# Kernel tuning notes

Hardware: AMD Instinct MI355X
Metric: run time of the kernel (lower is better)

## Reference

```python
import jax, jax.numpy as jnp
import numpy as np

P = 8          # patch_num_in == patch_num_out
R = 16         # patch_resolution (pixels per patch side)
C = 2          # dim_channel
D = 512        # dim_token
NH = 8         # nhead
DFF = 2048     # dim_feedforward
L = 6          # num_layers
PAIRS = 5      # demo_num
BS = 8
HW = P * R     # 128
S = PAIRS * 2 * P * P  # 640 tokens
EPS = 1e-5


def _patchify(x):
    # x: (N, c, H, W) -> (N, P*P, c*R*R)
    N, c, H, W = x.shape
    x = x.reshape(N, c, P, R, P, R).transpose(0, 2, 4, 1, 3, 5)
    return x.reshape(N, P * P, c * R * R)


def _depatchify(x, c):
    # x: (N, P*P, c*R*R) -> (N, c, P*R, P*R)
    N = x.shape[0]
    x = x.reshape(N, P, P, c, R, R).transpose(0, 3, 1, 4, 2, 5)
    return x.reshape(N, c, P * R, P * R)


def _ln(x, s, b):
    mu = jnp.mean(x, axis=-1, keepdims=True)
    var = jnp.mean(jnp.square(x - mu), axis=-1, keepdims=True)
    return (x - mu) * jax.lax.rsqrt(var + EPS) * s + b


def _block_lowtri_additive_mask(seq_len):
    blk = jnp.arange(seq_len) // (P * P)  # alternating init/end blocks of size P*P
    allowed = blk[:, None] >= blk[None, :]
    return jnp.where(allowed, 0.0, -jnp.inf).astype(jnp.float32)


def setup_inputs() -> dict:
    key = jax.random.key(0)
    ks = jax.random.split(key, 20)
    s = 0.02
    f32 = jnp.float32
    inp = {
        "init": jax.random.normal(ks[0], (BS, PAIRS, C, HW, HW), f32),
        "end": jax.random.normal(ks[1], (BS, PAIRS, C, HW, HW), f32),
        "c_mask": jnp.ones((BS, C), dtype=bool),
        "pre_W": (jax.random.normal(ks[2], (D, C * R * R), f32) * s),
        "pre_b": jnp.zeros((D,), f32),
        "post_W": (jax.random.normal(ks[3], (C * R * R, D), f32) * s),
        "post_b": jnp.zeros((C * R * R,), f32),
        "patch_pos": jax.random.normal(ks[4], (P * P, D), f32),
        "func_pos": jax.random.normal(ks[5], (PAIRS * 2, D), f32),
        "Wqkv": (jax.random.normal(ks[6], (L, 3 * D, D), f32) * s),
        "bqkv": jnp.zeros((L, 3 * D), f32),
        "Wo": (jax.random.normal(ks[7], (L, D, D), f32) * s),
        "bo": jnp.zeros((L, D), f32),
        "ln1_s": jnp.ones((L, D), f32),
        "ln1_b": jnp.zeros((L, D), f32),
        "ln2_s": jnp.ones((L, D), f32),
        "ln2_b": jnp.zeros((L, D), f32),
        "W1": (jax.random.normal(ks[8], (L, DFF, D), f32) * s),
        "b1": jnp.zeros((L, DFF), f32),
        "W2": (jax.random.normal(ks[9], (L, D, DFF), f32) * s),
        "b2": jnp.zeros((L, D), f32),
    }
    return inp


def _forward(init, end, pre_W, pre_b, post_W, post_b, patch_pos, func_pos,
             Wqkv, bqkv, Wo, bo, ln1_s, ln1_b, ln2_s, ln2_b, W1, b1, W2, b2):
    bs, pairs = init.shape[0], init.shape[1]
    # interleave (init, end) per pair: (bs, pairs, 2, c, h, w)
    x = jnp.concatenate([init[:, :, None], end[:, :, None]], axis=2)
    f = x.reshape(-1, C, HW, HW)
    f = _patchify(f)                                    # (N, P*P, C*R*R)
    f = f @ pre_W.T + pre_b                             # (N, P*P, D)
    f = f + patch_pos                                   # patch pos encoding
    f = f.reshape(bs, pairs * 2, P * P, D)
    f = f + func_pos[: pairs * 2][None, :, None, :]     # func pos encoding
    seq = pairs * 2 * P * P
    f = f.reshape(bs, seq, D)

    amask = _block_lowtri_additive_mask(seq)            # (S, S) additive
    dh = D // NH
    scale = 1.0 / np.sqrt(dh).astype(np.float32)

    for l in range(L):
        qkv = f @ Wqkv[l].T + bqkv[l]                   # (bs, S, 3D)
        q, k, v = jnp.split(qkv, 3, axis=-1)
        q = q.reshape(bs, seq, NH, dh).transpose(0, 2, 1, 3)
        k = k.reshape(bs, seq, NH, dh).transpose(0, 2, 1, 3)
        v = v.reshape(bs, seq, NH, dh).transpose(0, 2, 1, 3)
        scores = jnp.einsum('bhqd,bhkd->bhqk', q, k) * scale + amask
        attn = jax.nn.softmax(scores, axis=-1)
        o = jnp.einsum('bhqk,bhkd->bhqd', attn, v)
        o = o.transpose(0, 2, 1, 3).reshape(bs, seq, D)
        o = o @ Wo[l].T + bo[l]
        f = _ln(f + o, ln1_s[l], ln1_b[l])              # post-norm (PyTorch default)
        ff = jax.nn.gelu(f @ W1[l].T + b1[l], approximate=False) @ W2[l].T + b2[l]
        f = _ln(f + ff, ln2_s[l], ln2_b[l])

    f = f.reshape(bs, pairs, 2, P * P, D)[:, :, 0]      # read prediction off init slots
    f = f @ post_W.T + post_b                           # (bs, pairs, P*P, C*R*R)
    f = f.reshape(bs * pairs, P * P, C * R * R)
    f = _depatchify(f, C)
    return f.reshape(bs, pairs, C, HW, HW)


def reference(init, end, c_mask, pre_W, pre_b, post_W, post_b, patch_pos, func_pos,
              Wqkv, bqkv, Wo, bo, ln1_s, ln1_b, ln2_s, ln2_b, W1, b1, W2, b2):
    # c_mask is unpacked but unused by the original forward
    return _forward(init, end, pre_W, pre_b, post_W, post_b, patch_pos, func_pos,
                    Wqkv, bqkv, Wo, bo, ln1_s, ln1_b, ln2_s, ln2_b, W1, b1, W2, b2)
```

## Files before the change

kernel.cpp:

```cpp
#include <hip/hip_runtime.h>
#include <hip/hip_bf16.h>

#define BSZ 8
#define PAIRS 5
#define NCH 2
#define HWP 128
#define PP 64
#define DIM 512
#define NHEAD 8
#define DHEAD 64
#define DFF 2048
#define NLAYER 6
#define SEQ 640
#define NTOK (BSZ * SEQ)
#define FIN 10
#define MPOST (BSZ * PAIRS * PP)

typedef unsigned short u16;
typedef __bf16 bf16_t;
typedef __attribute__((ext_vector_type(8))) __bf16 bf16x8;
typedef __attribute__((ext_vector_type(4))) float f32x4;
#define MFMA16(a, b, c) __builtin_amdgcn_mfma_f32_16x16x32_bf16(a, b, c, 0, 0, 0)

__device__ __forceinline__ u16 f2b(float x) {
  unsigned u = __float_as_uint(x);
  return (u16)((u + 0x7fffu + ((u >> 16) & 1u)) >> 16);
}

__device__ __forceinline__ float gelu_t(float x) {
  float y = 0.7978845608f * (x + 0.044715f * x * x * x);
  y = fminf(fmaxf(y, -10.f), 10.f);
  float e = __expf(2.f * y);
  return 0.5f * x * (1.f + (e - 1.f) / (e + 1.f));
}

__device__ __forceinline__ void dma16(const u16* g, void* l) {
  __builtin_amdgcn_global_load_lds(
      (const __attribute__((address_space(1))) void*)g,
      (__attribute__((address_space(3))) void*)l, 16, 0, 0);
}

#define W_QKV (3 * DIM * DIM)
#define W_O (DIM * DIM)
#define W_1 (DFF * DIM)
#define OFF_O W_QKV
#define OFF_1 (W_QKV + W_O)
#define OFF_2 (W_QKV + W_O + W_1)
#define W_ALL (W_QKV + W_O + 2 * W_1)
#define PREPOST (2 * DIM * DIM)
#define N_CVT (PREPOST + NLAYER * W_ALL)

__global__ __launch_bounds__(256) void k_cvt_all(const float* __restrict__ preW,
                                                 const float* __restrict__ postW,
                                                 const float* __restrict__ wq,
                                                 const float* __restrict__ wo,
                                                 const float* __restrict__ w1,
                                                 const float* __restrict__ w2,
                                                 u16* __restrict__ dst) {
  int i = blockIdx.x * 256 + threadIdx.x;
  float v;
  if (i < DIM * DIM) v = preW[i];
  else if (i < PREPOST) v = postW[i - DIM * DIM];
  else {
    int j = i - PREPOST;
    int l = j / W_ALL;
    int r = j - l * W_ALL;
    if (r < OFF_O) v = wq[(size_t)l * W_QKV + r];
    else if (r < OFF_1) v = wo[(size_t)l * W_O + r - OFF_O];
    else if (r < OFF_2) v = w1[(size_t)l * W_1 + r - OFF_1];
    else v = w2[(size_t)l * W_1 + r - OFF_2];
  }
  dst[i] = f2b(v);
}

__global__ __launch_bounds__(256) void k_patchify(const float* __restrict__ init,
                                                  const float* __restrict__ endp,
                                                  u16* __restrict__ A) {
  int i = blockIdx.x * 256 + threadIdx.x;
  int d = i & 511;
  int g = i >> 9;
  int p = g & 63;
  int fi = (g >> 6) % FIN;
  int b = g / SEQ;
  int e = fi & 1;
  int pr = fi >> 1;
  int c = d >> 8;
  int r1 = (d >> 4) & 15;
  int r2 = d & 15;
  int row = ((p >> 3) << 4) + r1;
  int col = ((p & 7) << 4) + r2;
  const float* src = e ? endp : init;
  size_t off = ((size_t)((b * PAIRS + pr) * NCH + c) << 14) + (size_t)row * HWP + col;
  A[i] = f2b(src[off]);
}

template <int NT, int MODE>
__global__ __launch_bounds__(256) void k_mma(const u16* __restrict__ A,
                                             const u16* __restrict__ B,
                                             const float* __restrict__ bias,
                                             u16* __restrict__ outB,
                                             float* __restrict__ outP,
                                             float* __restrict__ outF,
                                             const float* __restrict__ pp,
                                             const float* __restrict__ fp,
                                             int M, int N, int K, int Kblk, int act) {
  constexpr int FJ = NT / 32;
  constexpr int NC = (4 + NT / 16) / 4;
  __shared__ __align__(16) bf16_t As[2][64][32];
  __shared__ __align__(16) bf16_t Bs[2][NT][32];
  const int t = threadIdx.x;
  const int w = t >> 6, lane = t & 63, quad = lane >> 4, l16 = lane & 15;
  int bx = blockIdx.x, by = blockIdx.y;
  if ((gridDim.y & 7) == 0) {
    int lin = bx + gridDim.x * by;
    int YT = gridDim.y >> 3;
    int xcd = lin & 7, slot = lin >> 3;
    by = xcd * YT + slot % YT;
    bx = slot / YT;
  }
  const int row0 = by << 6, col0 = bx * NT;
  const size_t kOff = (size_t)blockIdx.z * Kblk;
  const int mB = (w & 1) << 5;
  const int nB = (w >> 1) * (NT / 2);

  const u16* aP[4];
#pragma unroll
  for (int c = 0; c < 4; ++c) {
    int r = row0 + c * 16 + (lane >> 2);
    int g = r;
    if (MODE == 3) {
      int p = r & 63, pr = (r >> 6) % PAIRS, b = r / (PAIRS * PP);
      g = b * SEQ + pr * 128 + p;
    }
    aP[c] = A + (size_t)g * K + kOff + ((lane & 3) << 3);
  }
  const u16* bP = B + (size_t)(col0 + (lane >> 2)) * K + kOff + ((lane & 3) << 3);

  f32x4 acc[2][FJ];
#pragma unroll
  for (int i = 0; i < 2; ++i)
#pragma unroll
    for (int j = 0; j < FJ; ++j) acc[i][j] = (f32x4){0.f, 0.f, 0.f, 0.f};

  auto stage = [&](int bu, int kk) {
#pragma unroll
    for (int s = 0; s < NC; ++s) {
      int c = NC * w + s;
      if (c < 4) dma16(aP[c] + kk, &As[bu][c * 16][0]);
      else dma16(bP + (size_t)((c - 4) * 16) * K + kk, &Bs[bu][(c - 4) * 16][0]);
    }
  };

  const int iters = Kblk >> 5;
  stage(0, 0);
  for (int it = 0; it < iters; ++it) {
    const int cur = it & 1;
    if (it > 0) asm volatile("s_barrier" ::: "memory");
    const bool more = (it + 1 < iters);
    if (more) stage(cur ^ 1, (it + 1) << 5);
    if (more) {
      if (NC == 3) asm volatile("s_waitcnt vmcnt(3)" ::: "memory");
      else asm volatile("s_waitcnt vmcnt(2)" ::: "memory");
    } else {
      asm volatile("s_waitcnt vmcnt(0)" ::: "memory");
    }
    asm volatile("s_barrier" ::: "memory");
    bf16x8 af[2], bfr[FJ];
#pragma unroll
    for (int i = 0; i < 2; ++i)
      af[i] = *(const bf16x8*)&As[cur][mB + i * 16 + l16][quad * 8];
#pragma unroll
    for (int j = 0; j < FJ; ++j)
      bfr[j] = *(const bf16x8*)&Bs[cur][nB + j * 16 + l16][quad * 8];
#pragma unroll
    for (int i = 0; i < 2; ++i)
#pragma unroll
      for (int j = 0; j < FJ; ++j) acc[i][j] = MFMA16(af[i], bfr[j], acc[i][j]);
  }

#pragma unroll
  for (int i = 0; i < 2; ++i)
#pragma unroll
    for (int reg = 0; reg < 4; ++reg) {
      int m = row0 + mB + i * 16 + quad * 4 + reg;
#pragma unroll
      for (int j = 0; j < FJ; ++j) {
        int n = col0 + nB + j * 16 + l16;
        float v = acc[i][j][reg];
        if (MODE == 0) {
          v += bias[n];
          if (act) v = gelu_t(v);
          outB[(size_t)m * N + n] = f2b(v);
        } else if (MODE == 1) {
          outP[(size_t)blockIdx.z * M * N + (size_t)m * N + n] = v;
        } else if (MODE == 2) {
          int p = m & 63, fi = (m >> 6) % FIN;
          v += bias[n] + pp[p * DIM + n] + fp[fi * DIM + n];
          outF[(size_t)m * N + n] = v;
          outB[(size_t)m * N + n] = f2b(v);
        } else {
          v += bias[n];
          int p = m & 63, pr = (m >> 6) % PAIRS, b = m / (PAIRS * PP);
          int c = n >> 8, r1 = (n >> 4) & 15, r2 = n & 15;
          int row = ((p >> 3) << 4) + r1, col = ((p & 7) << 4) + r2;
          size_t off = ((size_t)((b * PAIRS + pr) * NCH + c) << 14) +
                       (size_t)row * HWP + col;
          outF[off] = v;
        }
      }
    }
}

__global__ __launch_bounds__(256) void k_attn(const u16* __restrict__ qkv,
                                              u16* __restrict__ o) {
  __shared__ bf16_t Qs[64][72];
  __shared__ bf16_t Ks[64][72];
  __shared__ bf16_t Vs[64][72];
  __shared__ bf16_t Ps[64][72];
  const int t = threadIdx.x;
  const int w = t >> 6, lane = t & 63, quad = lane >> 4, l16 = lane & 15;
  const int qblk = blockIdx.x, h = blockIdx.y, b = blockIdx.z;
  const int q0 = qblk << 6;
  const u16* base = qkv + (size_t)b * SEQ * (3 * DIM);
  const int sr = t >> 2;
  const int sd = (t & 3) << 4;
  {
    const u16* qp = base + (size_t)(q0 + sr) * (3 * DIM) + h * DHEAD + sd;
    *(bf16x8*)&Qs[sr][sd] = *(const bf16x8*)(const void*)qp;
    *(bf16x8*)&Qs[sr][sd + 8] = *(const bf16x8*)(const void*)(qp + 8);
  }
  __syncthreads();
  bf16x8 aQ0 = *(const bf16x8*)&Qs[w * 16 + l16][quad * 8];
  bf16x8 aQ1 = *(const bf16x8*)&Qs[w * 16 + l16][32 + quad * 8];
  f32x4 accO[4];
#pragma unroll
  for (int j = 0; j < 4; ++j) accO[j] = (f32x4){0.f, 0.f, 0.f, 0.f};
  float mSt[4] = {-1e30f, -1e30f, -1e30f, -1e30f};
  float lSt[4] = {0.f, 0.f, 0.f, 0.f};
  const int ntile = qblk + 1;
  for (int kt = 0; kt < ntile; ++kt) {
    {
      const u16* kp = base + (size_t)(kt * 64 + sr) * (3 * DIM) + DIM + h * DHEAD + sd;
      *(bf16x8*)&Ks[sr][sd] = *(const bf16x8*)(const void*)kp;
      *(bf16x8*)&Ks[sr][sd + 8] = *(const bf16x8*)(const void*)(kp + 8);
      const u16* vp = base + (size_t)(kt * 64 + sr) * (3 * DIM) + 2 * DIM + h * DHEAD + sd;
      bf16x8 v0 = *(const bf16x8*)(const void*)vp;
      bf16x8 v1 = *(const bf16x8*)(const void*)(vp + 8);
#pragma unroll
      for (int e = 0; e < 8; ++e) Vs[sd + e][sr] = v0[e];
#pragma unroll
      for (int e = 0; e < 8; ++e) Vs[sd + 8 + e][sr] = v1[e];
    }
    __syncthreads();
    f32x4 s[4];
#pragma unroll
    for (int j = 0; j < 4; ++j) {
      bf16x8 b0 = *(const bf16x8*)&Ks[j * 16 + l16][quad * 8];
      bf16x8 b1 = *(const bf16x8*)&Ks[j * 16 + l16][32 + quad * 8];
      s[j] = (f32x4){0.f, 0.f, 0.f, 0.f};
      s[j] = MFMA16(aQ0, b0, s[j]);
      s[j] = MFMA16(aQ1, b1, s[j]);
      s[j] *= 0.125f;
    }
#pragma unroll
    for (int reg = 0; reg < 4; ++reg) {
      float mx = fmaxf(fmaxf(s[0][reg], s[1][reg]), fmaxf(s[2][reg], s[3][reg]));
      mx = fmaxf(mx, __shfl_xor(mx, 1));
      mx = fmaxf(mx, __shfl_xor(mx, 2));
      mx = fmaxf(mx, __shfl_xor(mx, 4));
      mx = fmaxf(mx, __shfl_xor(mx, 8));
      float mNew = fmaxf(mSt[reg], mx);
      float alpha = __expf(mSt[reg] - mNew);
      mSt[reg] = mNew;
      float rs = 0.f;
#pragma unroll
      for (int j = 0; j < 4; ++j) {
        float p = __expf(s[j][reg] - mNew);
        s[j][reg] = p;
        rs += p;
      }
      rs += __shfl_xor(rs, 1);
      rs += __shfl_xor(rs, 2);
      rs += __shfl_xor(rs, 4);
      rs += __shfl_xor(rs, 8);
      lSt[reg] = lSt[reg] * alpha + rs;
#pragma unroll
      for (int j = 0; j < 4; ++j) accO[j][reg] *= alpha;
    }
#pragma unroll
    for (int j = 0; j < 4; ++j)
#pragma unroll
      for (int reg = 0; reg < 4; ++reg)
        *(u16*)&Ps[w * 16 + quad * 4 + reg][j * 16 + l16] = f2b(s[j][reg]);
    __syncthreads();
    bf16x8 aP0 = *(const bf16x8*)&Ps[w * 16 + l16][quad * 8];
    bf16x8 aP1 = *(const bf16x8*)&Ps[w * 16 + l16][32 + quad * 8];
#pragma unroll
    for (int jd = 0; jd < 4; ++jd) {
      bf16x8 b0 = *(const bf16x8*)&Vs[jd * 16 + l16][quad * 8];
      bf16x8 b1 = *(const bf16x8*)&Vs[jd * 16 + l16][32 + quad * 8];
      accO[jd] = MFMA16(aP0, b0, accO[jd]);
      accO[jd] = MFMA16(aP1, b1, accO[jd]);
    }
    __syncthreads();
  }
#pragma unroll
  for (int reg = 0; reg < 4; ++reg) {
    float inv = 1.0f / lSt[reg];
    int row = q0 + w * 16 + quad * 4 + reg;
#pragma unroll
    for (int jd = 0; jd < 4; ++jd)
      o[((size_t)(b * SEQ + row)) * DIM + h * DHEAD + jd * 16 + l16] =
          f2b(accO[jd][reg] * inv);
  }
}

__global__ __launch_bounds__(256) void k_red_ln(const float* __restrict__ part, int KS,
                                                const float* __restrict__ bias,
                                                float* __restrict__ f,
                                                u16* __restrict__ fb,
                                                const float* __restrict__ s,
                                                const float* __restrict__ bvec) {
  const int row = blockIdx.x;
  const int t = threadIdx.x;
  const size_t base = (size_t)row * DIM;
  float x0 = f[base + t] + bias[t];
  float x1 = f[base + t + 256] + bias[t + 256];
  for (int z = 0; z < KS; ++z) {
    x0 += part[(size_t)z * NTOK * DIM + base + t];
    x1 += part[(size_t)z * NTOK * DIM + base + t + 256];
  }
  float sum = x0 + x1;
  float sq = x0 * x0 + x1 * x1;
#pragma unroll
  for (int off = 32; off; off >>= 1) {
    sum += __shfl_xor(sum, off);
    sq += __shfl_xor(sq, off);
  }
  __shared__ float rs[4], rq[4];
  const int w = t >> 6, lane = t & 63;
  if (lane == 0) { rs[w] = sum; rq[w] = sq; }
  __syncthreads();
  float tot = rs[0] + rs[1] + rs[2] + rs[3];
  float tq2 = rq[0] + rq[1] + rq[2] + rq[3];
  float mu = tot * (1.0f / 512.0f);
  float var = tq2 * (1.0f / 512.0f) - mu * mu;
  float rstd = rsqrtf(var + 1e-5f);
  float v0 = (x0 - mu) * rstd * s[t] + bvec[t];
  float v1 = (x1 - mu) * rstd * s[t + 256] + bvec[t + 256];
  f[base + t] = v0;
  f[base + t + 256] = v1;
  fb[base + t] = f2b(v0);
  fb[base + t + 256] = f2b(v1);
}

extern "C" void kernel_launch(void* const* d_in, const int* in_sizes, int n_in,
                              void* d_out, int out_size, void* d_ws, size_t ws_size,
                              hipStream_t stream) {
  const float* init = (const float*)d_in[0];
  const float* endp = (const float*)d_in[1];
  const float* pre_W = (const float*)d_in[3];
  const float* pre_b = (const float*)d_in[4];
  const float* post_W = (const float*)d_in[5];
  const float* post_b = (const float*)d_in[6];
  const float* patch_pos = (const float*)d_in[7];
  const float* func_pos = (const float*)d_in[8];
  const float* Wqkv = (const float*)d_in[9];
  const float* bqkv = (const float*)d_in[10];
  const float* Wo = (const float*)d_in[11];
  const float* bo = (const float*)d_in[12];
  const float* ln1_s = (const float*)d_in[13];
  const float* ln1_b = (const float*)d_in[14];
  const float* ln2_s = (const float*)d_in[15];
  const float* ln2_b = (const float*)d_in[16];
  const float* W1 = (const float*)d_in[17];
  const float* b1 = (const float*)d_in[18];
  const float* W2 = (const float*)d_in[19];
  const float* b2 = (const float*)d_in[20];
  float* out = (float*)d_out;

  char* p = (char*)d_ws;
  float* buf_f = (float*)p;    p += (size_t)NTOK * DIM * 4;
  u16* buf_fb = (u16*)p;       p += (size_t)NTOK * DIM * 2;
  u16* buf_attn = (u16*)p;     p += (size_t)NTOK * DIM * 2;
  u16* shared_b = (u16*)p;     p += (size_t)NTOK * DFF * 2;
  u16* wAll = (u16*)p;         p += (size_t)N_CVT * 2;
  float* partial = (float*)p;
  u16* buf_patch = shared_b;
  u16* buf_qkv = shared_b;
  u16* buf_hid = shared_b;
  u16* wPre = wAll;
  u16* wPost = wAll + DIM * DIM;
  u16* wL = wAll + PREPOST;

  dim3 blk(256);
  const int elems = NTOK * DIM;

  k_cvt_all<<<N_CVT / 256, blk, 0, stream>>>(pre_W, post_W, Wqkv, Wo, W1, W2, wAll);
  k_patchify<<<elems / 256, blk, 0, stream>>>(init, endp, buf_patch);
  k_mma<64, 2><<<dim3(8, 80, 1), blk, 0, stream>>>(
      buf_patch, wPre, pre_b, buf_fb, nullptr, buf_f, patch_pos, func_pos,
      NTOK, DIM, DIM, DIM, 0);

  for (int l = 0; l < NLAYER; ++l) {
    u16* wB = wL + (size_t)l * W_ALL;
    k_mma<128, 0><<<dim3(12, 80, 1), blk, 0, stream>>>(
        buf_fb, wB, bqkv + (size_t)l * 3 * DIM, buf_qkv, nullptr, nullptr, nullptr,
        nullptr, NTOK, 3 * DIM, DIM, DIM, 0);
    k_attn<<<dim3(SEQ / 64, NHEAD, BSZ), blk, 0, stream>>>(buf_qkv, buf_attn);
    k_mma<64, 1><<<dim3(8, 80, 1), blk, 0, stream>>>(
        buf_attn, wB + OFF_O, nullptr, nullptr, partial, nullptr, nullptr, nullptr,
        NTOK, DIM, DIM, DIM, 0);
    k_red_ln<<<NTOK, blk, 0, stream>>>(partial, 1, bo + (size_t)l * DIM, buf_f,
                                       buf_fb, ln1_s + (size_t)l * DIM,
                                       ln1_b + (size_t)l * DIM);
    k_mma<128, 0><<<dim3(16, 80, 1), blk, 0, stream>>>(
        buf_fb, wB + OFF_1, b1 + (size_t)l * DFF, buf_hid, nullptr, nullptr, nullptr,
        nullptr, NTOK, DFF, DIM, DIM, 1);
    k_mma<64, 1><<<dim3(8, 80, 2), blk, 0, stream>>>(
        buf_hid, wB + OFF_2, nullptr, nullptr, partial, nullptr, nullptr, nullptr,
        NTOK, DIM, DFF, DFF / 2, 0);
    k_red_ln<<<NTOK, blk, 0, stream>>>(partial, 2, b2 + (size_t)l * DIM, buf_f,
                                       buf_fb, ln2_s + (size_t)l * DIM,
                                       ln2_b + (size_t)l * DIM);
  }

  k_mma<64, 3><<<dim3(8, 40, 1), blk, 0, stream>>>(
      buf_fb, wPost, post_b, nullptr, nullptr, out, nullptr, nullptr,
      MPOST, DIM, DIM, DIM, 0);
}
```

Measured before the change: 972.6 us.

## Triple-buffer GEMM loads, prefetch attention K/V, vectorize weight cast, drop FFN2 split-K

The GEMM mainloop goes from double to triple buffering in LDS, issuing async loads two K-steps ahead with adjusted vmcnt waits, to hide more global latency. The attention kernel now prefetches the next K/V tile into registers while the current tile is processed. The weight conversion kernel handles 8 elements per thread with vector loads and stores. The FFN down-projection drops its 2-way split-K, so there are fewer partials to reduce but only half as many blocks for that GEMM.

```diff
diff --git a/kernel.cpp b/kernel.cpp
--- a/kernel.cpp
+++ b/kernel.cpp
@@ -19,6 +19,7 @@
 typedef unsigned short u16;
 typedef __bf16 bf16_t;
 typedef __attribute__((ext_vector_type(8))) __bf16 bf16x8;
+typedef __attribute__((ext_vector_type(8))) unsigned short u16x8;
 typedef __attribute__((ext_vector_type(4))) float f32x4;
 #define MFMA16(a, b, c) __builtin_amdgcn_mfma_f32_16x16x32_bf16(a, b, c, 0, 0, 0)
 
@@ -57,20 +58,26 @@
                                                  const float* __restrict__ w1,
                                                  const float* __restrict__ w2,
                                                  u16* __restrict__ dst) {
-  int i = blockIdx.x * 256 + threadIdx.x;
-  float v;
-  if (i < DIM * DIM) v = preW[i];
-  else if (i < PREPOST) v = postW[i - DIM * DIM];
+  size_t i = ((size_t)blockIdx.x * 256 + threadIdx.x) * 8;
+  const float* src;
+  size_t off;
+  if (i < DIM * DIM) { src = preW; off = i; }
+  else if (i < PREPOST) { src = postW; off = i - DIM * DIM; }
   else {
-    int j = i - PREPOST;
-    int l = j / W_ALL;
-    int r = j - l * W_ALL;
-    if (r < OFF_O) v = wq[(size_t)l * W_QKV + r];
-    else if (r < OFF_1) v = wo[(size_t)l * W_O + r - OFF_O];
-    else if (r < OFF_2) v = w1[(size_t)l * W_1 + r - OFF_1];
-    else v = w2[(size_t)l * W_1 + r - OFF_2];
-  }
-  dst[i] = f2b(v);
+    size_t j = i - PREPOST;
+    int l = (int)(j / W_ALL);
+    size_t r = j - (size_t)l * W_ALL;
+    if (r < OFF_O) { src = wq + (size_t)l * W_QKV; off = r; }
+    else if (r < OFF_1) { src = wo + (size_t)l * W_O; off = r - OFF_O; }
+    else if (r < OFF_2) { src = w1 + (size_t)l * W_1; off = r - OFF_1; }
+    else { src = w2 + (size_t)l * W_1; off = r - OFF_2; }
+  }
+  float4 v0 = *(const float4*)(src + off);
+  float4 v1 = *(const float4*)(src + off + 4);
+  u16x8 o;
+  o[0] = f2b(v0.x); o[1] = f2b(v0.y); o[2] = f2b(v0.z); o[3] = f2b(v0.w);
+  o[4] = f2b(v1.x); o[5] = f2b(v1.y); o[6] = f2b(v1.z); o[7] = f2b(v1.w);
+  *(u16x8*)(dst + i) = o;
 }
 
 __global__ __launch_bounds__(256) void k_patchify(const float* __restrict__ init,
@@ -106,8 +113,8 @@
                                              int M, int N, int K, int Kblk, int act) {
   constexpr int FJ = NT / 32;
   constexpr int NC = (4 + NT / 16) / 4;
-  __shared__ __align__(16) bf16_t As[2][64][32];
-  __shared__ __align__(16) bf16_t Bs[2][NT][32];
+  __shared__ __align__(16) bf16_t As[3][64][32];
+  __shared__ __align__(16) bf16_t Bs[3][NT][32];
   const int t = threadIdx.x;
   const int w = t >> 6, lane = t & 63, quad = lane >> 4, l16 = lane & 15;
   int bx = blockIdx.x, by = blockIdx.y;
@@ -153,12 +160,15 @@
 
   const int iters = Kblk >> 5;
   stage(0, 0);
+  stage(1, 32);
   for (int it = 0; it < iters; ++it) {
-    const int cur = it & 1;
+    const int cur = it % 3;
     if (it > 0) asm volatile("s_barrier" ::: "memory");
-    const bool more = (it + 1 < iters);
-    if (more) stage(cur ^ 1, (it + 1) << 5);
-    if (more) {
+    if (it + 2 < iters) stage((it + 2) % 3, (it + 2) << 5);
+    if (it + 2 < iters) {
+      if (NC == 3) asm volatile("s_waitcnt vmcnt(6)" ::: "memory");
+      else asm volatile("s_waitcnt vmcnt(4)" ::: "memory");
+    } else if (it + 1 < iters) {
       if (NC == 3) asm volatile("s_waitcnt vmcnt(3)" ::: "memory");
       else asm volatile("s_waitcnt vmcnt(2)" ::: "memory");
     } else {
@@ -224,8 +234,9 @@
   const u16* base = qkv + (size_t)b * SEQ * (3 * DIM);
   const int sr = t >> 2;
   const int sd = (t & 3) << 4;
+  const int rowB = 3 * DIM;
   {
-    const u16* qp = base + (size_t)(q0 + sr) * (3 * DIM) + h * DHEAD + sd;
+    const u16* qp = base + (size_t)(q0 + sr) * rowB + h * DHEAD + sd;
     *(bf16x8*)&Qs[sr][sd] = *(const bf16x8*)(const void*)qp;
     *(bf16x8*)&Qs[sr][sd + 8] = *(const bf16x8*)(const void*)(qp + 8);
   }
@@ -238,18 +249,26 @@
   float mSt[4] = {-1e30f, -1e30f, -1e30f, -1e30f};
   float lSt[4] = {0.f, 0.f, 0.f, 0.f};
   const int ntile = qblk + 1;
+  const u16* kp0 = base + (size_t)sr * rowB + DIM + h * DHEAD + sd;
+  const u16* vp0 = base + (size_t)sr * rowB + 2 * DIM + h * DHEAD + sd;
+  bf16x8 kR0 = *(const bf16x8*)(const void*)kp0;
+  bf16x8 kR1 = *(const bf16x8*)(const void*)(kp0 + 8);
+  bf16x8 vR0 = *(const bf16x8*)(const void*)vp0;
+  bf16x8 vR1 = *(const bf16x8*)(const void*)(vp0 + 8);
   for (int kt = 0; kt < ntile; ++kt) {
-    {
-      const u16* kp = base + (size_t)(kt * 64 + sr) * (3 * DIM) + DIM + h * DHEAD + sd;
-      *(bf16x8*)&Ks[sr][sd] = *(const bf16x8*)(const void*)kp;
-      *(bf16x8*)&Ks[sr][sd + 8] = *(const bf16x8*)(const void*)(kp + 8);
-      const u16* vp = base + (size_t)(kt * 64 + sr) * (3 * DIM) + 2 * DIM + h * DHEAD + sd;
-      bf16x8 v0 = *(const bf16x8*)(const void*)vp;
-      bf16x8 v1 = *(const bf16x8*)(const void*)(vp + 8);
-#pragma unroll
-      for (int e = 0; e < 8; ++e) Vs[sd + e][sr] = v0[e];
-#pragma unroll
-      for (int e = 0; e < 8; ++e) Vs[sd + 8 + e][sr] = v1[e];
+    *(bf16x8*)&Ks[sr][sd] = kR0;
+    *(bf16x8*)&Ks[sr][sd + 8] = kR1;
+#pragma unroll
+    for (int e = 0; e < 8; ++e) Vs[sd + e][sr] = vR0[e];
+#pragma unroll
+    for (int e = 0; e < 8; ++e) Vs[sd + 8 + e][sr] = vR1[e];
+    if (kt + 1 < ntile) {
+      const u16* kp = kp0 + (size_t)(kt + 1) * 64 * rowB;
+      const u16* vp = vp0 + (size_t)(kt + 1) * 64 * rowB;
+      kR0 = *(const bf16x8*)(const void*)kp;
+      kR1 = *(const bf16x8*)(const void*)(kp + 8);
+      vR0 = *(const bf16x8*)(const void*)vp;
+      vR1 = *(const bf16x8*)(const void*)(vp + 8);
     }
     __syncthreads();
     f32x4 s[4];
@@ -396,7 +415,8 @@
   dim3 blk(256);
   const int elems = NTOK * DIM;
 
-  k_cvt_all<<<N_CVT / 256, blk, 0, stream>>>(pre_W, post_W, Wqkv, Wo, W1, W2, wAll);
+  k_cvt_all<<<N_CVT / (256 * 8), blk, 0, stream>>>(pre_W, post_W, Wqkv, Wo, W1, W2,
+                                                   wAll);
   k_patchify<<<elems / 256, blk, 0, stream>>>(init, endp, buf_patch);
   k_mma<64, 2><<<dim3(8, 80, 1), blk, 0, stream>>>(
       buf_patch, wPre, pre_b, buf_fb, nullptr, buf_f, patch_pos, func_pos,
@@ -417,10 +437,10 @@
     k_mma<128, 0><<<dim3(16, 80, 1), blk, 0, stream>>>(
         buf_fb, wB + OFF_1, b1 + (size_t)l * DFF, buf_hid, nullptr, nullptr, nullptr,
         nullptr, NTOK, DFF, DIM, DIM, 1);
-    k_mma<64, 1><<<dim3(8, 80, 2), blk, 0, stream>>>(
+    k_mma<64, 1><<<dim3(8, 80, 1), blk, 0, stream>>>(
         buf_hid, wB + OFF_2, nullptr, nullptr, partial, nullptr, nullptr, nullptr,
-        NTOK, DIM, DFF, DFF / 2, 0);
-    k_red_ln<<<NTOK, blk, 0, stream>>>(partial, 2, b2 + (size_t)l * DIM, buf_f,
+        NTOK, DIM, DFF, DFF, 0);
+    k_red_ln<<<NTOK, blk, 0, stream>>>(partial, 1, b2 + (size_t)l * DIM, buf_f,
                                        buf_fb, ln2_s + (size_t)l * DIM,
                                        ln2_b + (size_t)l * DIM);
   }
```

Measured after the change: 943.2 us. 1.03x faster.
